# Performance work log

Hardware: AMD Instinct MI355X
Metric: run time of the kernel (lower is better)

Reference implementation:

```python
import jax, jax.numpy as jnp
from jax import lax
import numpy as np

I_SIZE = 1024
H_SIZE = 1024
BATCH = 64
SEQ = 512


def _xavier(key, shape):
    # matches nn.init.xavier_uniform_ for 2D params
    fan_in, fan_out = shape
    limit = float(np.sqrt(6.0 / (fan_in + fan_out)))
    return jax.random.uniform(key, shape, jnp.float32, -limit, limit)


def setup_inputs() -> dict:
    key = jax.random.key(0)
    ks = jax.random.split(key, 9)
    x = jax.random.normal(ks[0], (BATCH, SEQ, I_SIZE), jnp.float32)
    w_ii = _xavier(ks[1], (I_SIZE, H_SIZE))
    w_hi = _xavier(ks[2], (H_SIZE, H_SIZE))
    w_if = _xavier(ks[3], (I_SIZE, H_SIZE))
    w_hf = _xavier(ks[4], (H_SIZE, H_SIZE))
    w_ig = _xavier(ks[5], (I_SIZE, H_SIZE))
    w_hg = _xavier(ks[6], (H_SIZE, H_SIZE))
    w_io = _xavier(ks[7], (I_SIZE, H_SIZE))
    w_ho = _xavier(ks[8], (H_SIZE, H_SIZE))
    zb = jnp.zeros((H_SIZE,), jnp.float32)  # init_hidden zeros all 1D params
    return {
        "x": x,
        "w_ii": w_ii, "b_ii": zb, "w_hi": w_hi, "b_hi": zb,
        "w_if": w_if, "b_if": zb, "w_hf": w_hf, "b_hf": zb,
        "w_ig": w_ig, "b_ig": zb, "w_hg": w_hg, "b_hg": zb,
        "w_io": w_io, "b_io": zb, "w_ho": w_ho, "b_ho": zb,
    }


def reference(x, w_ii, b_ii, w_hi, b_hi, w_if, b_if, w_hf, b_hf,
              w_ig, b_ig, w_hg, b_hg, w_io, b_io, w_ho, b_ho):
    # Fuse the 4 input-side and 4 hidden-side GEMMs into one each (same math).
    Wi = jnp.concatenate([w_ii, w_if, w_ig, w_io], axis=1)        # (I, 4H)
    Wh = jnp.concatenate([w_hi, w_hf, w_hg, w_ho], axis=1)        # (H, 4H)
    b = jnp.concatenate([b_ii + b_hi, b_if + b_hf, b_ig + b_hg, b_io + b_ho])  # (4H,)
    # Precompute all input projections in one big GEMM: (B, S, 4H)
    x_proj = jnp.einsum('bsi,ih->bsh', x, Wi) + b

    B = x.shape[0]
    H = w_hi.shape[0]
    h0 = jnp.zeros((B, H), x.dtype)

    def step(carry, xt):
        h, c = carry
        gates = xt + h @ Wh                       # (B, 4H)
        i, f, g, o = jnp.split(gates, 4, axis=-1)
        i = jax.nn.sigmoid(i)
        f = jax.nn.sigmoid(f)
        g = jnp.tanh(g)
        o = jax.nn.sigmoid(o)
        c = c * f + i * g
        h = o * jnp.tanh(c)
        return (h, c), None

    (h_t, c_t), _ = lax.scan(step, (h0, h0), jnp.swapaxes(x_proj, 0, 1))
    return (h_t, c_t)
```

## Files before the change

### kernel.cpp

```cpp
#include <hip/hip_runtime.h>


typedef __bf16 bf16x8 __attribute__((ext_vector_type(8)));
typedef float f32x4 __attribute__((ext_vector_type(4)));
typedef unsigned int uint4v __attribute__((ext_vector_type(4)));

__device__ __forceinline__ unsigned short f2bf(float f) {
    unsigned int u = __float_as_uint(f);
    u = (u + 0x7FFFu + ((u >> 16) & 1u)) >> 16;
    return (unsigned short)u;
}
__device__ __forceinline__ float bf2f(unsigned short u) {
    return __uint_as_float((unsigned int)u << 16);
}

__global__ __launch_bounds__(256) void pack_wT(
    const float* __restrict__ w0, const float* __restrict__ w1,
    const float* __restrict__ w2, const float* __restrict__ w3,
    const float* __restrict__ w4, const float* __restrict__ w5,
    const float* __restrict__ w6, const float* __restrict__ w7,
    unsigned short* __restrict__ wiT, unsigned short* __restrict__ whT)
{
    __shared__ float tl[64][65];
    int bid = blockIdx.x;
    int mi = bid >> 8;
    int tile = bid & 255;
    int tk = tile >> 4, tj = tile & 15;
    const float* w;
    int gate = mi & 3;
    if (mi < 4) w = (gate == 0) ? w0 : (gate == 1) ? w1 : (gate == 2) ? w2 : w3;
    else        w = (gate == 0) ? w4 : (gate == 1) ? w5 : (gate == 2) ? w6 : w7;
    unsigned short* out = (mi < 4) ? wiT : whT;
    int tx = threadIdx.x & 63, ty = threadIdx.x >> 6;
    #pragma unroll
    for (int i = 0; i < 16; i++) {
        int k = i * 4 + ty;
        tl[k][tx] = w[(long)(tk * 64 + k) * 1024 + tj * 64 + tx];
    }
    __syncthreads();
    #pragma unroll
    for (int i = 0; i < 16; i++) {
        int j = i * 4 + ty;
        out[(long)(gate * 1024 + tj * 64 + j) * 1024 + tk * 64 + tx] = f2bf(tl[tx][j]);
    }
}

__global__ __launch_bounds__(256) void pack_misc(
    const float* __restrict__ bi0, const float* __restrict__ bh0,
    const float* __restrict__ bi1, const float* __restrict__ bh1,
    const float* __restrict__ bi2, const float* __restrict__ bh2,
    const float* __restrict__ bi3, const float* __restrict__ bh3,
    float* __restrict__ bias, unsigned int* __restrict__ hbuf_u,
    unsigned int* __restrict__ flags)
{
    int idx = blockIdx.x * 256 + threadIdx.x;
    hbuf_u[idx] = 0u;
    if (idx < 4096) {
        int g = idx >> 10, j = idx & 1023;
        const float* bi = (g == 0) ? bi0 : (g == 1) ? bi1 : (g == 2) ? bi2 : bi3;
        const float* bh = (g == 0) ? bh0 : (g == 1) ? bh1 : (g == 2) ? bh2 : bh3;
        bias[idx] = bi[j] + bh[j];
    }
    if (idx < 256) flags[idx] = 0u;
}

__global__ __launch_bounds__(256, 2) void gemm_xproj(
    const float* __restrict__ x, const unsigned short* __restrict__ wiT,
    unsigned short* __restrict__ xp)
{
    __shared__ unsigned short sA[128 * 72];
    __shared__ unsigned short sB[128 * 72];
    int bid = blockIdx.x;
    int mt = bid >> 5, nt = bid & 31;
    long m0 = (long)mt * 128;
    int n0 = nt * 128;
    int tid = threadIdx.x;
    int lane = tid & 63, wv = tid >> 6;
    int quad = lane >> 4, l15 = lane & 15;
    int wm = wv & 1, wn = wv >> 1;

    f32x4 acc[4][4];
    #pragma unroll
    for (int a = 0; a < 4; a++)
        #pragma unroll
        for (int b = 0; b < 4; b++)
            acc[a][b] = (f32x4){0.f, 0.f, 0.f, 0.f};

    for (int kb = 0; kb < 16; kb++) {
        int k0 = kb * 64;
        #pragma unroll
        for (int i = 0; i < 8; i++) {
            int ch = tid + i * 256;
            int row = ch >> 4, q = ch & 15;
            float4 v = *(const float4*)&x[(m0 + row) * 1024 + k0 + q * 4];
            uint2 p;
            p.x = (unsigned int)f2bf(v.x) | ((unsigned int)f2bf(v.y) << 16);
            p.y = (unsigned int)f2bf(v.z) | ((unsigned int)f2bf(v.w) << 16);
            *(uint2*)&sA[row * 72 + q * 4] = p;
        }
        #pragma unroll
        for (int i = 0; i < 4; i++) {
            int ch = tid + i * 256;
            int row = ch >> 3, q = ch & 7;
            uint4 v = *(const uint4*)&wiT[(long)(n0 + row) * 1024 + k0 + q * 8];
            *(uint4*)&sB[row * 72 + q * 8] = v;
        }
        __syncthreads();
        #pragma unroll
        for (int ks = 0; ks < 2; ks++) {
            bf16x8 af[4], bfr[4];
            #pragma unroll
            for (int mi2 = 0; mi2 < 4; mi2++)
                af[mi2] = *(const bf16x8*)&sA[(wm * 64 + mi2 * 16 + l15) * 72 + ks * 32 + quad * 8];
            #pragma unroll
            for (int ni = 0; ni < 4; ni++)
                bfr[ni] = *(const bf16x8*)&sB[(wn * 64 + ni * 16 + l15) * 72 + ks * 32 + quad * 8];
            #pragma unroll
            for (int mi2 = 0; mi2 < 4; mi2++)
                #pragma unroll
                for (int ni = 0; ni < 4; ni++)
                    acc[mi2][ni] = __builtin_amdgcn_mfma_f32_16x16x32_bf16(
                        af[mi2], bfr[ni], acc[mi2][ni], 0, 0, 0);
        }
        __syncthreads();
    }
    #pragma unroll
    for (int mi2 = 0; mi2 < 4; mi2++)
        #pragma unroll
        for (int ni = 0; ni < 4; ni++)
            #pragma unroll
            for (int r = 0; r < 4; r++) {
                long row = m0 + wm * 64 + mi2 * 16 + quad * 4 + r;
                int col = n0 + wn * 64 + ni * 16 + l15;
                int h = col & 1023, gate = col >> 10;
                xp[row * 4096 + h * 4 + gate] = f2bf(acc[mi2][ni][r]);
            }
}

__global__ __launch_bounds__(256, 2) void lstm_scan(
    const unsigned short* __restrict__ xp, const unsigned short* __restrict__ whT,
    const float* __restrict__ bias, unsigned short* __restrict__ hbuf,
    unsigned int* __restrict__ flags, float* __restrict__ out)
{
    __shared__ unsigned short hl[16 * 1032];
    __shared__ float xch[4][16][16];

    int bid = blockIdx.x;
    int g = bid >> 6, s = bid & 63;
    int tid = threadIdx.x;
    int lane = tid & 63, wv = tid >> 6;
    int quad = lane >> 4, l15 = lane & 15;

    bf16x8 bfrag[32];
    {
        const unsigned short* bp = whT + (long)(wv * 1024 + s * 16 + l15) * 1024 + quad * 8;
        #pragma unroll
        for (int kk = 0; kk < 32; kk++)
            bfrag[kk] = *(const bf16x8*)(bp + kk * 32);
    }

    int row = tid >> 4, col = tid & 15;
    float b4[4];
    #pragma unroll
    for (int gg = 0; gg < 4; gg++) b4[gg] = bias[gg * 1024 + s * 16 + col];

    float c = 0.f;
    const unsigned int* myflags = flags + g * 64 + lane;
    unsigned int* myflag = flags + g * 64 + s;
    const char* hb0 = (const char*)(hbuf + g * 16 * 1024);
    const char* hb1 = (const char*)(hbuf + 4 * 16 * 1024 + g * 16 * 1024);
    unsigned short* hw0 = hbuf + g * 16 * 1024;
    unsigned short* hw1 = hbuf + 4 * 16 * 1024 + g * 16 * 1024;

    for (int t = 0; t < 512; t++) {
        const unsigned short* xr = xp + ((long)(g * 16 + row) * 512 + t) * 4096
                                      + (s * 16 + col) * 4;
        uint2 xg = *(const uint2*)xr;
        float xpi = bf2f((unsigned short)(xg.x & 0xFFFF));
        float xpf = bf2f((unsigned short)(xg.x >> 16));
        float xpg = bf2f((unsigned short)(xg.y & 0xFFFF));
        float xpo = bf2f((unsigned short)(xg.y >> 16));

        if (t > 0) {
            while (true) {
                unsigned int f = __hip_atomic_load(myflags, __ATOMIC_RELAXED,
                                                   __HIP_MEMORY_SCOPE_AGENT);
                if (__all((int)(f >= (unsigned int)t))) break;
                __builtin_amdgcn_s_sleep(1);
            }
        }

        const char* hsrc = (t & 1) ? hb1 : hb0;
        uint4v hv[8];
        #pragma unroll
        for (int i = 0; i < 8; i++) {
            int ch = tid + i * 256;
            int r2 = ch >> 7, off = ch & 127;
            const void* p = hsrc + r2 * 2048 + off * 16;
            asm volatile("global_load_dwordx4 %0, %1, off sc0 sc1"
                         : "=v"(hv[i]) : "v"(p) : "memory");
        }
        asm volatile("s_waitcnt vmcnt(0)" ::: "memory");
        #pragma unroll
        for (int i = 0; i < 8; i++) {
            int ch = tid + i * 256;
            int r2 = ch >> 7, off = ch & 127;
            *(uint4v*)&hl[r2 * 1032 + off * 8] = hv[i];
        }
        __syncthreads();

        f32x4 acc = {0.f, 0.f, 0.f, 0.f};
        #pragma unroll
        for (int kk = 0; kk < 32; kk++) {
            bf16x8 af = *(const bf16x8*)&hl[l15 * 1032 + kk * 32 + quad * 8];
            acc = __builtin_amdgcn_mfma_f32_16x16x32_bf16(af, bfrag[kk], acc, 0, 0, 0);
        }
        #pragma unroll
        for (int r = 0; r < 4; r++)
            xch[wv][quad * 4 + r][l15] = acc[r];
        __syncthreads();

        float gi = xch[0][row][col] + xpi + b4[0];
        float gf = xch[1][row][col] + xpf + b4[1];
        float gg_ = xch[2][row][col] + xpg + b4[2];
        float go = xch[3][row][col] + xpo + b4[3];
        float iv = 1.f / (1.f + __expf(-gi));
        float fv = 1.f / (1.f + __expf(-gf));
        float gv = 1.f - 2.f / (__expf(2.f * gg_) + 1.f);
        float ov = 1.f / (1.f + __expf(-go));
        c = c * fv + iv * gv;
        float h = ov * (1.f - 2.f / (__expf(2.f * c) + 1.f));

        if (t == 511) {
            out[(g * 16 + row) * 1024 + s * 16 + col] = h;
            out[65536 + (g * 16 + row) * 1024 + s * 16 + col] = c;
        } else {
            unsigned short* hdst = (t & 1) ? hw0 : hw1;
            __hip_atomic_store(&hdst[row * 1024 + s * 16 + col], f2bf(h),
                               __ATOMIC_RELAXED, __HIP_MEMORY_SCOPE_AGENT);
            __syncthreads();
            if (tid == 0)
                __hip_atomic_store(myflag, (unsigned int)(t + 1),
                                   __ATOMIC_RELAXED, __HIP_MEMORY_SCOPE_AGENT);
        }
    }
}

extern "C" void kernel_launch(void* const* d_in, const int* in_sizes, int n_in,
                              void* d_out, int out_size, void* d_ws, size_t ws_size,
                              hipStream_t stream)
{
    const float* x    = (const float*)d_in[0];
    const float* w_ii = (const float*)d_in[1];
    const float* b_ii = (const float*)d_in[2];
    const float* w_hi = (const float*)d_in[3];
    const float* b_hi = (const float*)d_in[4];
    const float* w_if = (const float*)d_in[5];
    const float* b_if = (const float*)d_in[6];
    const float* w_hf = (const float*)d_in[7];
    const float* b_hf = (const float*)d_in[8];
    const float* w_ig = (const float*)d_in[9];
    const float* b_ig = (const float*)d_in[10];
    const float* w_hg = (const float*)d_in[11];
    const float* b_hg = (const float*)d_in[12];
    const float* w_io = (const float*)d_in[13];
    const float* b_io = (const float*)d_in[14];
    const float* w_ho = (const float*)d_in[15];
    const float* b_ho = (const float*)d_in[16];

    const size_t OFF_XPJ  = 0;
    const size_t OFF_WIT  = 268435456;
    const size_t OFF_WHT  = 276824064;
    const size_t OFF_BIAS = 285212672;
    const size_t OFF_HBUF = 285229056;
    const size_t OFF_FLG  = 285491200;
    const size_t NEEDED   = 285493248;
    if (ws_size < NEEDED) return;

    char* ws = (char*)d_ws;
    unsigned short* xpj      = (unsigned short*)(ws + OFF_XPJ);
    unsigned short* wiT      = (unsigned short*)(ws + OFF_WIT);
    unsigned short* whT      = (unsigned short*)(ws + OFF_WHT);
    float*          bias     = (float*)(ws + OFF_BIAS);
    unsigned short* hbuf     = (unsigned short*)(ws + OFF_HBUF);
    unsigned int*   flags    = (unsigned int*)(ws + OFF_FLG);

    pack_wT<<<2048, 256, 0, stream>>>(w_ii, w_if, w_ig, w_io,
                                      w_hi, w_hf, w_hg, w_ho, wiT, whT);
    pack_misc<<<256, 256, 0, stream>>>(b_ii, b_hi, b_if, b_hf, b_ig, b_hg, b_io, b_ho,
                                       bias, (unsigned int*)hbuf, flags);
    gemm_xproj<<<8192, 256, 0, stream>>>(x, wiT, xpj);
    lstm_scan<<<256, 256, 0, stream>>>(xpj, whT, bias, hbuf, flags, (float*)d_out);
}
```

Before: 2.385 ms.

## Repartition LSTM scan into 8-row batch groups with 32-column slices per block

Changes the recurrent scan decomposition from 4 batch groups × 64 column slices (16 rows, 16 cols per block) to 8 groups × 32 slices (8 batch rows, 32 hidden columns per block). Each block holds two register-resident weight tiles and issues two MFMAs per k-step, but half the MFMA rows are wasted because only 8 batch rows exist. Each block loads half as much h from global memory, and each group's flag barrier spans 32 blocks instead of 64, which should shorten the per-step synchronisation. The cost is doubled weight registers, with launch bounds relaxed to one block per CU, and wasted MFMA throughput. The launch grid presumably stays at 256 blocks.

```diff
diff --git a/kernel.cpp b/kernel.cpp
--- a/kernel.cpp
+++ b/kernel.cpp
@@ -137,44 +137,47 @@
             }
 }
 
-__global__ __launch_bounds__(256, 2) void lstm_scan(
+__global__ __launch_bounds__(256, 1) void lstm_scan(
     const unsigned short* __restrict__ xp, const unsigned short* __restrict__ whT,
     const float* __restrict__ bias, unsigned short* __restrict__ hbuf,
     unsigned int* __restrict__ flags, float* __restrict__ out)
 {
-    __shared__ unsigned short hl[16 * 1032];
-    __shared__ float xch[4][16][16];
+    __shared__ unsigned short hl[8 * 1032];
+    __shared__ float xch[4][8][32];
 
     int bid = blockIdx.x;
-    int g = bid >> 6, s = bid & 63;
+    int g = bid >> 5, s = bid & 31;
     int tid = threadIdx.x;
     int lane = tid & 63, wv = tid >> 6;
     int quad = lane >> 4, l15 = lane & 15;
-
-    bf16x8 bfrag[32];
-    {
-        const unsigned short* bp = whT + (long)(wv * 1024 + s * 16 + l15) * 1024 + quad * 8;
+    int arow = l15 & 7;
+
+    bf16x8 bfrag[2][32];
+    #pragma unroll
+    for (int ti = 0; ti < 2; ti++) {
+        const unsigned short* bp =
+            whT + (long)(wv * 1024 + s * 32 + ti * 16 + l15) * 1024 + quad * 8;
         #pragma unroll
         for (int kk = 0; kk < 32; kk++)
-            bfrag[kk] = *(const bf16x8*)(bp + kk * 32);
-    }
-
-    int row = tid >> 4, col = tid & 15;
+            bfrag[ti][kk] = *(const bf16x8*)(bp + kk * 32);
+    }
+
+    int row = tid >> 5, col = tid & 31;
     float b4[4];
     #pragma unroll
-    for (int gg = 0; gg < 4; gg++) b4[gg] = bias[gg * 1024 + s * 16 + col];
+    for (int gg = 0; gg < 4; gg++) b4[gg] = bias[gg * 1024 + s * 32 + col];
 
     float c = 0.f;
-    const unsigned int* myflags = flags + g * 64 + lane;
-    unsigned int* myflag = flags + g * 64 + s;
-    const char* hb0 = (const char*)(hbuf + g * 16 * 1024);
-    const char* hb1 = (const char*)(hbuf + 4 * 16 * 1024 + g * 16 * 1024);
-    unsigned short* hw0 = hbuf + g * 16 * 1024;
-    unsigned short* hw1 = hbuf + 4 * 16 * 1024 + g * 16 * 1024;
+    const unsigned int* myflags = flags + g * 32 + (lane & 31);
+    unsigned int* myflag = flags + g * 32 + s;
+    const char* hb0 = (const char*)(hbuf + (long)g * 8 * 1024);
+    const char* hb1 = (const char*)(hbuf + 65536 + (long)g * 8 * 1024);
+    unsigned short* hw0 = hbuf + (long)g * 8 * 1024;
+    unsigned short* hw1 = hbuf + 65536 + (long)g * 8 * 1024;
 
     for (int t = 0; t < 512; t++) {
-        const unsigned short* xr = xp + ((long)(g * 16 + row) * 512 + t) * 4096
-                                      + (s * 16 + col) * 4;
+        const unsigned short* xr = xp + ((long)(g * 8 + row) * 512 + t) * 4096
+                                      + (s * 32 + col) * 4;
         uint2 xg = *(const uint2*)xr;
         float xpi = bf2f((unsigned short)(xg.x & 0xFFFF));
         float xpf = bf2f((unsigned short)(xg.x >> 16));
@@ -191,9 +194,9 @@
         }
 
         const char* hsrc = (t & 1) ? hb1 : hb0;
-        uint4v hv[8];
-        #pragma unroll
-        for (int i = 0; i < 8; i++) {
+        uint4v hv[4];
+        #pragma unroll
+        for (int i = 0; i < 4; i++) {
             int ch = tid + i * 256;
             int r2 = ch >> 7, off = ch & 127;
             const void* p = hsrc + r2 * 2048 + off * 16;
@@ -202,22 +205,28 @@
         }
         asm volatile("s_waitcnt vmcnt(0)" ::: "memory");
         #pragma unroll
-        for (int i = 0; i < 8; i++) {
+        for (int i = 0; i < 4; i++) {
             int ch = tid + i * 256;
             int r2 = ch >> 7, off = ch & 127;
             *(uint4v*)&hl[r2 * 1032 + off * 8] = hv[i];
         }
         __syncthreads();
 
-        f32x4 acc = {0.f, 0.f, 0.f, 0.f};
+        f32x4 acc0 = {0.f, 0.f, 0.f, 0.f};
+        f32x4 acc1 = {0.f, 0.f, 0.f, 0.f};
         #pragma unroll
         for (int kk = 0; kk < 32; kk++) {
-            bf16x8 af = *(const bf16x8*)&hl[l15 * 1032 + kk * 32 + quad * 8];
-            acc = __builtin_amdgcn_mfma_f32_16x16x32_bf16(af, bfrag[kk], acc, 0, 0, 0);
-        }
-        #pragma unroll
-        for (int r = 0; r < 4; r++)
-            xch[wv][quad * 4 + r][l15] = acc[r];
+            bf16x8 af = *(const bf16x8*)&hl[arow * 1032 + kk * 32 + quad * 8];
+            acc0 = __builtin_amdgcn_mfma_f32_16x16x32_bf16(af, bfrag[0][kk], acc0, 0, 0, 0);
+            acc1 = __builtin_amdgcn_mfma_f32_16x16x32_bf16(af, bfrag[1][kk], acc1, 0, 0, 0);
+        }
+        if (quad < 2) {
+            #pragma unroll
+            for (int r = 0; r < 4; r++) {
+                xch[wv][quad * 4 + r][l15] = acc0[r];
+                xch[wv][quad * 4 + r][16 + l15] = acc1[r];
+            }
+        }
         __syncthreads();
 
         float gi = xch[0][row][col] + xpi + b4[0];
@@ -232,11 +241,11 @@
         float h = ov * (1.f - 2.f / (__expf(2.f * c) + 1.f));
 
         if (t == 511) {
-            out[(g * 16 + row) * 1024 + s * 16 + col] = h;
-            out[65536 + (g * 16 + row) * 1024 + s * 16 + col] = c;
+            out[(g * 8 + row) * 1024 + s * 32 + col] = h;
+            out[65536 + (g * 8 + row) * 1024 + s * 32 + col] = c;
         } else {
             unsigned short* hdst = (t & 1) ? hw0 : hw1;
-            __hip_atomic_store(&hdst[row * 1024 + s * 16 + col], f2bf(h),
+            __hip_atomic_store(&hdst[row * 1024 + s * 32 + col], f2bf(h),
                                __ATOMIC_RELAXED, __HIP_MEMORY_SCOPE_AGENT);
             __syncthreads();
             if (tid == 0)
```

Result: faster. 2.056 ms (-13.8%).
